# Kernel optimization log

Measured on AMD Instinct MI355X. Metric: run time of the kernel, lower is better.

The kernel has to match this reference:

```python
import jax, jax.numpy as jnp
import numpy as np

NEG_INF = -1e9  # large negative used to mask the H-direction self position (CCNet INF trick)


def _cca(x, q_w, q_b, k_w, k_b, v_w, v_b, gamma):
    # x: [B, C, H, W]
    B, C, H, W = x.shape
    # 1x1 convs are per-pixel channel matmuls
    q = jnp.einsum('oc,bchw->bohw', q_w, x) + q_b[None, :, None, None]  # [B,2,H,W]
    k = jnp.einsum('oc,bchw->bohw', k_w, x) + k_b[None, :, None, None]  # [B,2,H,W]
    v = jnp.einsum('oc,bchw->bohw', v_w, x) + v_b[None, :, None, None]  # [B,16,H,W]

    # column (H-direction) affinities: query (h,w) vs keys (j,w)
    energy_H = jnp.einsum('bchw,bcjw->bhwj', q, k)  # [B,H,W,H]
    diag = jnp.eye(H, dtype=bool)[None, :, None, :]  # mask j == h (self counted once, in W branch)
    energy_H = jnp.where(diag, NEG_INF, energy_H)
    # row (W-direction) affinities: query (h,w) vs keys (h,j)
    energy_W = jnp.einsum('bchw,bchj->bhwj', q, k)  # [B,H,W,W]

    attn = jax.nn.softmax(jnp.concatenate([energy_H, energy_W], axis=3), axis=3)  # [B,H,W,H+W]
    att_H = attn[..., :H]
    att_W = attn[..., H:]

    out_H = jnp.einsum('bhwj,bcjw->bchw', att_H, v)
    out_W = jnp.einsum('bhwj,bchj->bchw', att_W, v)
    return gamma[0] * (out_H + out_W) + x


def setup_inputs() -> dict:
    key = jax.random.key(0)
    ks = jax.random.split(key, 8)
    b, c, d, h, w = 1, 16, 24, 96, 192
    return {
        'cost_volume': jax.random.normal(ks[0], (b, c, d, h, w), jnp.float32),
        'q_w': jax.random.normal(ks[1], (2, 16), jnp.float32) * 0.1,
        'q_b': jax.random.normal(ks[2], (2,), jnp.float32) * 0.1,
        'k_w': jax.random.normal(ks[3], (2, 16), jnp.float32) * 0.1,
        'k_b': jax.random.normal(ks[4], (2,), jnp.float32) * 0.1,
        'v_w': jax.random.normal(ks[5], (16, 16), jnp.float32) * 0.1,
        'v_b': jax.random.normal(ks[6], (16,), jnp.float32) * 0.1,
        'gamma': jax.random.normal(ks[7], (1,), jnp.float32),
    }


def reference(cost_volume, q_w, q_b, k_w, k_b, v_w, v_b, gamma):
    b, c, d, h, w = cost_volume.shape
    # fold disparity into batch: [b,c,d,h,w] -> [b*d, c, h, w]
    x = jnp.transpose(cost_volume, (0, 2, 1, 3, 4)).reshape(b * d, c, h, w)
    x = _cca(x, q_w, q_b, k_w, k_b, v_w, v_b, gamma)
    x = _cca(x, q_w, q_b, k_w, k_b, v_w, v_b, gamma)  # same module applied twice
    return jnp.transpose(x.reshape(b, d, c, h, w), (0, 2, 1, 3, 4))
```

## Files before the change

kernel.cpp:

```cpp
#include <hip/hip_runtime.h>

#define C 16
#define NIMG 24
#define H 96
#define W 192
#define PX (H*W)
#define LOG2E 1.44269504088896f

typedef float v2f  __attribute__((ext_vector_type(2)));
typedef float v4f  __attribute__((ext_vector_type(4)));
typedef short v8s  __attribute__((ext_vector_type(8)));

#define QP_OFF 0
#define KP_OFF (NIMG*PX*2)
#define VB4_OFF (2*NIMG*PX*2)
#define VBP_OFF (VB4_OFF + NIMG*PX*C/2)
#define CMAX_OFF (VBP_OFF + NIMG*PX*C/2)
#define RMAX_OFF (CMAX_OFF + NIMG*2*W)
#define SC_OFF   (RMAX_OFF + NIMG*2*H)
#define ACC_OFF  (SC_OFF + NIMG*PX)

__device__ __forceinline__ unsigned short f2bf(float x) {
    union { float f; unsigned u; } v; v.f = x;
    unsigned r = v.u + 0x7fffu + ((v.u >> 16) & 1u);
    return (unsigned short)(r >> 16);
}
__device__ __forceinline__ float bf2f(unsigned short u) {
    union { unsigned u; float f; } v; v.u = ((unsigned)u) << 16;
    return v.f;
}

__global__ __launch_bounds__(256)
void qkv_kernel(const float* __restrict__ x, long xn_s, long xc_s,
                const float* __restrict__ qw, const float* __restrict__ qb,
                const float* __restrict__ kw, const float* __restrict__ kb,
                const float* __restrict__ vw, const float* __restrict__ vb,
                float2* __restrict__ Qp, float2* __restrict__ Kp,
                ushort4* __restrict__ Vb4, unsigned short* __restrict__ Vbp,
                float* __restrict__ cmax_zero)
{
    __shared__ float wq[2*C+2], wk[2*C+2], wv[C*C+C];
    int tid = threadIdx.x;
    if (tid < 2*C) { wq[tid] = qw[tid]; wk[tid] = kw[tid]; }
    if (tid < 2)   { wq[2*C+tid] = qb[tid]; wk[2*C+tid] = kb[tid]; }
    if (tid < C*C) wv[tid] = vw[tid];
    if (tid < C)   wv[C*C+tid] = vb[tid];

    if (blockIdx.x < 36) {
        int zi = blockIdx.x*256 + tid;
        if (zi < NIMG*2*W) cmax_zero[zi] = 0.0f;
    }
    __syncthreads();

    int id = blockIdx.x*256 + tid;
    int n  = id / PX;
    int p  = id - n*PX;
    int h  = p / W;
    int w  = p - h*W;
    const float* xp = x + (long)n*xn_s + p;

    float xv[C];
    #pragma unroll
    for (int c = 0; c < C; c++) xv[c] = xp[(long)c*xc_s];

    float q0 = wq[2*C], q1 = wq[2*C+1];
    float k0 = wk[2*C], k1 = wk[2*C+1];
    #pragma unroll
    for (int c = 0; c < C; c++) {
        q0 += wq[c]*xv[c];   q1 += wq[C+c]*xv[c];
        k0 += wk[c]*xv[c];   k1 += wk[C+c]*xv[c];
    }
    Qp[id] = make_float2(q0, q1);
    Kp[id] = make_float2(k0, k1);

    float vv[C];
    #pragma unroll
    for (int o = 0; o < C; o++) {
        float a = wv[C*C+o];
        #pragma unroll
        for (int c = 0; c < C; c++) a += wv[o*C+c]*xv[c];
        vv[o] = a;
    }
    unsigned short vb16[C];
    #pragma unroll
    for (int o = 0; o < C; o++) vb16[o] = f2bf(vv[o]);

    #pragma unroll
    for (int c4 = 0; c4 < 4; c4++) {
        ushort4 u;
        u.x = vb16[c4*4+0]; u.y = vb16[c4*4+1];
        u.z = vb16[c4*4+2]; u.w = vb16[c4*4+3];
        Vb4[(((long)n*H + h)*4 + c4)*W + w] = u;
    }
    #pragma unroll
    for (int o = 0; o < C; o++)
        Vbp[(((long)n*H + h)*16 + o)*W + w] = vb16[o];
}

__global__ __launch_bounds__(192)
void stats_kernel(const float2* __restrict__ Kp,
                  float* __restrict__ cmax, float* __restrict__ rmax)
{
    int bid = blockIdx.x;
    int n   = bid >> 2;
    int h0  = (bid & 3) * 24;
    int tid = threadIdx.x;
    const float2* Kpn = Kp + n*PX;

    float c0 = 0.f, c1 = 0.f;
    #pragma unroll 4
    for (int h = 0; h < 24; h++) {
        float2 k = Kpn[(h0+h)*W + tid];
        c0 = fmaxf(c0, fabsf(k.x));
        c1 = fmaxf(c1, fabsf(k.y));
    }
    atomicMax((unsigned*)&cmax[n*2*W + tid],     __float_as_uint(c0));
    atomicMax((unsigned*)&cmax[n*2*W + W + tid], __float_as_uint(c1));

    int r = tid >> 3, seg = tid & 7;
    float r0 = 0.f, r1 = 0.f;
    const float2* kr = Kpn + (h0+r)*W + seg*24;
    #pragma unroll 4
    for (int j = 0; j < 24; j++) {
        float2 k = kr[j];
        r0 = fmaxf(r0, fabsf(k.x));
        r1 = fmaxf(r1, fabsf(k.y));
    }
    r0 = fmaxf(r0, __shfl_xor(r0, 1)); r0 = fmaxf(r0, __shfl_xor(r0, 2)); r0 = fmaxf(r0, __shfl_xor(r0, 4));
    r1 = fmaxf(r1, __shfl_xor(r1, 1)); r1 = fmaxf(r1, __shfl_xor(r1, 2)); r1 = fmaxf(r1, __shfl_xor(r1, 4));
    if (seg == 0) {
        rmax[n*2*H + h0 + r]     = r0;
        rmax[n*2*H + H + h0 + r] = r1;
    }
}

#define VT_WS 1672
__global__ __launch_bounds__(256)
void col_attn_kernel(const float2* __restrict__ Qp, const float2* __restrict__ Kp,
                     const ushort4* __restrict__ Vb4,
                     const float* __restrict__ cmax, const float* __restrict__ rmax,
                     unsigned short* __restrict__ accC, float* __restrict__ sC)
{
    __shared__ unsigned short Vt[4*VT_WS];
    __shared__ unsigned short Ks[4*2*96];
    __shared__ float2         Qs[4*96];
    __shared__ float          Ms[4*96];

    const int chunk = (NIMG*48) / 8;
    int bid = blockIdx.x;
    int swz = (bid & 7)*chunk + (bid >> 3);
    int n   = swz / 48;
    int wg  = swz - n*48;
    int w0  = wg*4;
    int tid = threadIdx.x;

    const float2* Qpn = Qp + n*PX;
    const float2* Kpn = Kp + n*PX;
    const ushort4* Vbn = Vb4 + (long)n*PX*4;

    #pragma unroll
    for (int i = 0; i < 6; i++) {
        int idx = i*256 + tid;
        int wl  = idx & 3;
        int c4  = (idx >> 2) & 3;
        int j   = idx >> 4;
        ushort4 v = Vbn[((long)j*4 + c4)*W + w0 + wl];
        int b = wl*VT_WS + (c4*4)*104 + j;
        Vt[b        ] = v.x;
        Vt[b + 104  ] = v.y;
        Vt[b + 208  ] = v.z;
        Vt[b + 312  ] = v.w;
    }
    #pragma unroll
    for (int i = 0; i < 2; i++) {
        int idx = i*256 + tid;
        if (idx < 384) {
            int wl = idx & 3;
            int j  = idx >> 2;
            float2 kk = Kpn[j*W + w0 + wl];
            Ks[wl*192 + j]      = f2bf(kk.x);
            Ks[wl*192 + 96 + j] = f2bf(kk.y);
        }
    }
    #pragma unroll
    for (int i = 0; i < 2; i++) {
        int idx = i*256 + tid;
        if (idx < 384) {
            int wl = idx & 3;
            int h  = idx >> 2;
            int w  = w0 + wl;
            float2 qq = Qpn[h*W + w];
            float qx = qq.x * LOG2E, qy = qq.y * LOG2E;
            float c0 = cmax[n*2*W + w], c1 = cmax[n*2*W + W + w];
            float r0 = rmax[n*2*H + h], r1 = rmax[n*2*H + H + h];
            float ax = fabsf(qx), ay = fabsf(qy);
            Qs[wl*96 + h] = make_float2(qx, qy);
            Ms[wl*96 + h] = fmaxf(ax*c0 + ay*c1, ax*r0 + ay*r1);
        }
    }
    __syncthreads();

    int wl   = tid >> 6;
    int lane = tid & 63;
    int li   = lane & 15;
    int g    = lane >> 4;
    int w    = w0 + wl;
    unsigned short* accCn = accC + (long)n*PX*16;

    #pragma unroll
    for (int ht = 0; ht < 6; ht++) {
        int hglob = ht*16 + li;
        float2 q = Qs[wl*96 + hglob];
        float  m = Ms[wl*96 + hglob];

        v4f acc = {};
        float sp = 0.f;
        #pragma unroll
        for (int kc = 0; kc < 3; kc++) {
            int j0 = kc*32 + g*8;
            v8s bv = *(const v8s*)&Vt[wl*VT_WS + li*104 + j0];
            v8s kxv = *(const v8s*)&Ks[wl*192 + j0];
            v8s kyv = *(const v8s*)&Ks[wl*192 + 96 + j0];
            v8s af;
            #pragma unroll
            for (int e = 0; e < 8; e++) {
                float e2 = bf2f((unsigned short)kxv[e])*q.x
                         + bf2f((unsigned short)kyv[e])*q.y - m;
                float p = __builtin_amdgcn_exp2f(e2);
                p = (j0 + e == hglob) ? 0.0f : p;
                sp += p;
                af[e] = (short)f2bf(p);
            }
            acc = __builtin_amdgcn_mfma_f32_16x16x32_bf16(af, bv, acc, 0, 0, 0);
        }
        sp += __shfl_xor(sp, 16);
        sp += __shfl_xor(sp, 32);
        if (lane < 16)
            sC[((long)n*H + hglob)*W + w] = sp;

        #pragma unroll
        for (int rr = 0; rr < 4; rr++) {
            int h2 = ht*16 + g*4 + rr;
            accCn[((long)h2*W + w)*16 + li] = f2bf(acc[rr]);
        }
    }
}

__global__ __launch_bounds__(256)
void row_attn_kernel(const float2* __restrict__ Qp, const float2* __restrict__ Kp,
                     const unsigned short* __restrict__ Vbp,
                     const float* __restrict__ cmax, const float* __restrict__ rmax,
                     const unsigned short* __restrict__ accC, const float* __restrict__ sC,
                     const float* __restrict__ xres, long xn_s, long xc_s,
                     float* __restrict__ out, long on_s, long oc_s,
                     const float* __restrict__ gamma_p)
{
    const int chunk = (NIMG*(H/2)) / 8;
    int bid = blockIdx.x;
    int swz = (bid & 7)*chunk + (bid >> 3);
    int n   = swz / (H/2);
    int h0  = (swz - n*(H/2)) * 2;
    int tid = threadIdx.x;

    const float2* Qpn = Qp + n*PX;
    const float*  Kf  = (const float*)(Kp + n*PX);
    const unsigned short* Vrn = Vbp + (long)n*PX*16;

    int wv   = tid >> 6;
    int r    = wv >> 1;
    int half = wv & 1;
    int lane = tid & 63;
    int li   = lane & 15;
    int g    = lane >> 4;
    int h    = h0 + r;

    float r0 = rmax[n*2*H + h], r1 = rmax[n*2*H + H + h];
    float qx[6], qy[6], mW[6];
    #pragma unroll
    for (int t = 0; t < 6; t++) {
        int w = (half*6 + t)*16 + li;
        float2 qq = Qpn[h*W + w];
        float c0 = cmax[n*2*W + w], c1 = cmax[n*2*W + W + w];
        float lqx = qq.x * LOG2E, lqy = qq.y * LOG2E;
        qx[t] = lqx; qy[t] = lqy;
        mW[t] = fmaxf(fabsf(lqx)*c0 + fabsf(lqy)*c1, fabsf(lqx)*r0 + fabsf(lqy)*r1);
    }

    v4f acc[6] = {};
    float sp[6] = {0.f,0.f,0.f,0.f,0.f,0.f};

    const unsigned short* Vrow = Vrn + (long)h*16*W + (long)li*W;
    const float*          Krow = Kf + (long)h*W*2;

    #pragma unroll
    for (int kc = 0; kc < 6; kc++) {
        int j0 = kc*32 + g*8;
        v8s af = *(const v8s*)(Vrow + j0);
        const v4f* kp4 = (const v4f*)(Krow + j0*2);
        v4f k0 = kp4[0], k1 = kp4[1], k2 = kp4[2], k3 = kp4[3];
        float kxv[8] = {k0[0],k0[2],k1[0],k1[2],k2[0],k2[2],k3[0],k3[2]};
        float kyv[8] = {k0[1],k0[3],k1[1],k1[3],k2[1],k2[3],k3[1],k3[3]};
        #pragma unroll
        for (int t = 0; t < 6; t++) {
            v8s bf;
            float sl = sp[t];
            #pragma unroll
            for (int e = 0; e < 8; e++) {
                float ev = qx[t]*kxv[e] + qy[t]*kyv[e];
                float p = __builtin_amdgcn_exp2f(ev - mW[t]);
                sl += p;
                bf[e] = (short)f2bf(p);
            }
            sp[t] = sl;
            acc[t] = __builtin_amdgcn_mfma_f32_16x16x32_bf16(af, bf, acc[t], 0, 0, 0);
        }
    }

    float gam = gamma_p[0];
    #pragma unroll
    for (int t = 0; t < 6; t++) {
        float s = sp[t];
        s += __shfl_xor(s, 16);
        s += __shfl_xor(s, 32);
        int w = (half*6 + t)*16 + li;
        float st = sC[((long)n*H + h)*W + w] + s;
        float inv = 1.0f / st;
        long po = (long)h*W + w;
        const unsigned short* cap = accC + (((long)n*H + h)*W + w)*16 + g*4;
        #pragma unroll
        for (int rr = 0; rr < 4; rr++) {
            int c = g*4 + rr;
            float ac = bf2f(cap[rr]);
            float tot = (acc[t][rr] + ac) * inv;
            out[(long)n*on_s + (long)c*oc_s + po] =
                gam*tot + xres[(long)n*xn_s + (long)c*xc_s + po];
        }
    }
}

extern "C" void kernel_launch(void* const* d_in, const int* in_sizes, int n_in,
                              void* d_out, int out_size, void* d_ws, size_t ws_size,
                              hipStream_t stream) {
    const float* cost = (const float*)d_in[0];
    const float* q_w  = (const float*)d_in[1];
    const float* q_b  = (const float*)d_in[2];
    const float* k_w  = (const float*)d_in[3];
    const float* k_b  = (const float*)d_in[4];
    const float* v_w  = (const float*)d_in[5];
    const float* v_b  = (const float*)d_in[6];
    const float* gamma= (const float*)d_in[7];
    float* out = (float*)d_out;
    float* ws  = (float*)d_ws;

    float2*  Qp = (float2*)(ws + QP_OFF);
    float2*  Kp = (float2*)(ws + KP_OFF);
    ushort4* Vb4 = (ushort4*)(ws + VB4_OFF);
    unsigned short* Vbp = (unsigned short*)(ws + VBP_OFF);
    float*   cm = ws + CMAX_OFF;
    float*   rm = ws + RMAX_OFF;
    float*   sC = ws + SC_OFF;
    unsigned short* aC = (unsigned short*)(ws + ACC_OFF);

    const int qkv_blocks  = (NIMG*PX)/256;
    const int stat_blocks = NIMG*4;
    const int col_blocks  = NIMG*48;
    const int row_blocks  = NIMG*(H/2);

    qkv_kernel<<<qkv_blocks, 256, 0, stream>>>(
        cost, (long)PX, (long)NIMG*PX,
        q_w, q_b, k_w, k_b, v_w, v_b, Qp, Kp, Vb4, Vbp, cm);
    stats_kernel<<<stat_blocks, 192, 0, stream>>>(Kp, cm, rm);
    col_attn_kernel<<<col_blocks, 256, 0, stream>>>(
        Qp, Kp, Vb4, cm, rm, aC, sC);
    row_attn_kernel<<<row_blocks, 256, 0, stream>>>(
        Qp, Kp, Vbp, cm, rm, aC, sC,
        cost, (long)PX, (long)NIMG*PX,
        out,  (long)PX, (long)NIMG*PX,
        gamma);

    qkv_kernel<<<qkv_blocks, 256, 0, stream>>>(
        out, (long)PX, (long)NIMG*PX,
        q_w, q_b, k_w, k_b, v_w, v_b, Qp, Kp, Vb4, Vbp, cm);
    stats_kernel<<<stat_blocks, 192, 0, stream>>>(Kp, cm, rm);
    col_attn_kernel<<<col_blocks, 256, 0, stream>>>(
        Qp, Kp, Vb4, cm, rm, aC, sC);
    row_attn_kernel<<<row_blocks, 256, 0, stream>>>(
        Qp, Kp, Vbp, cm, rm, aC, sC,
        out, (long)PX, (long)NIMG*PX,
        out, (long)PX, (long)NIMG*PX,
        gamma);
}
```

Before: 156.3 us.

## Fuse key-magnitude stats into QKV kernel using per-image global max bound

Drops the separate stats kernel. The QKV kernel now computes a per-image global max of |k| with wave shuffles and atomicMax, and both attention kernels form their softmax shift from that single bound instead of per-row and per-column maxima. The column kernel also stops staging Q and the bound in LDS and reads Q directly from global memory. This trades a coarser, looser exponent shift, which risks exp2 underflow and lost precision when key magnitudes vary a lot, for two fewer launches and less global traffic. The buffer is zeroed only once per call, so the second pass reuses a bound that already includes the first pass's values.

```diff
diff --git a/kernel.cpp b/kernel.cpp
--- a/kernel.cpp
+++ b/kernel.cpp
@@ -15,10 +15,9 @@
 #define KP_OFF (NIMG*PX*2)
 #define VB4_OFF (2*NIMG*PX*2)
 #define VBP_OFF (VB4_OFF + NIMG*PX*C/2)
-#define CMAX_OFF (VBP_OFF + NIMG*PX*C/2)
-#define RMAX_OFF (CMAX_OFF + NIMG*2*W)
-#define SC_OFF   (RMAX_OFF + NIMG*2*H)
-#define ACC_OFF  (SC_OFF + NIMG*PX)
+#define GM_OFF  (VBP_OFF + NIMG*PX*C/2)
+#define SC_OFF  (GM_OFF + 128)
+#define ACC_OFF (SC_OFF + NIMG*PX)
 
 __device__ __forceinline__ unsigned short f2bf(float x) {
     union { float f; unsigned u; } v; v.f = x;
@@ -37,7 +36,7 @@
                 const float* __restrict__ vw, const float* __restrict__ vb,
                 float2* __restrict__ Qp, float2* __restrict__ Kp,
                 ushort4* __restrict__ Vb4, unsigned short* __restrict__ Vbp,
-                float* __restrict__ cmax_zero)
+                float* __restrict__ gm)
 {
     __shared__ float wq[2*C+2], wk[2*C+2], wv[C*C+C];
     int tid = threadIdx.x;
@@ -45,11 +44,6 @@
     if (tid < 2)   { wq[2*C+tid] = qb[tid]; wk[2*C+tid] = kb[tid]; }
     if (tid < C*C) wv[tid] = vw[tid];
     if (tid < C)   wv[C*C+tid] = vb[tid];
-
-    if (blockIdx.x < 36) {
-        int zi = blockIdx.x*256 + tid;
-        if (zi < NIMG*2*W) cmax_zero[zi] = 0.0f;
-    }
     __syncthreads();
 
     int id = blockIdx.x*256 + tid;
@@ -73,6 +67,19 @@
     Qp[id] = make_float2(q0, q1);
     Kp[id] = make_float2(k0, k1);
 
+    {
+        float a0 = fabsf(k0), a1 = fabsf(k1);
+        #pragma unroll
+        for (int d = 1; d < 64; d <<= 1) {
+            a0 = fmaxf(a0, __shfl_xor(a0, d));
+            a1 = fmaxf(a1, __shfl_xor(a1, d));
+        }
+        if ((tid & 63) == 0) {
+            atomicMax((unsigned*)&gm[n*2+0], __float_as_uint(a0));
+            atomicMax((unsigned*)&gm[n*2+1], __float_as_uint(a1));
+        }
+    }
+
     float vv[C];
     #pragma unroll
     for (int o = 0; o < C; o++) {
@@ -97,54 +104,15 @@
         Vbp[(((long)n*H + h)*16 + o)*W + w] = vb16[o];
 }
 
-__global__ __launch_bounds__(192)
-void stats_kernel(const float2* __restrict__ Kp,
-                  float* __restrict__ cmax, float* __restrict__ rmax)
-{
-    int bid = blockIdx.x;
-    int n   = bid >> 2;
-    int h0  = (bid & 3) * 24;
-    int tid = threadIdx.x;
-    const float2* Kpn = Kp + n*PX;
-
-    float c0 = 0.f, c1 = 0.f;
-    #pragma unroll 4
-    for (int h = 0; h < 24; h++) {
-        float2 k = Kpn[(h0+h)*W + tid];
-        c0 = fmaxf(c0, fabsf(k.x));
-        c1 = fmaxf(c1, fabsf(k.y));
-    }
-    atomicMax((unsigned*)&cmax[n*2*W + tid],     __float_as_uint(c0));
-    atomicMax((unsigned*)&cmax[n*2*W + W + tid], __float_as_uint(c1));
-
-    int r = tid >> 3, seg = tid & 7;
-    float r0 = 0.f, r1 = 0.f;
-    const float2* kr = Kpn + (h0+r)*W + seg*24;
-    #pragma unroll 4
-    for (int j = 0; j < 24; j++) {
-        float2 k = kr[j];
-        r0 = fmaxf(r0, fabsf(k.x));
-        r1 = fmaxf(r1, fabsf(k.y));
-    }
-    r0 = fmaxf(r0, __shfl_xor(r0, 1)); r0 = fmaxf(r0, __shfl_xor(r0, 2)); r0 = fmaxf(r0, __shfl_xor(r0, 4));
-    r1 = fmaxf(r1, __shfl_xor(r1, 1)); r1 = fmaxf(r1, __shfl_xor(r1, 2)); r1 = fmaxf(r1, __shfl_xor(r1, 4));
-    if (seg == 0) {
-        rmax[n*2*H + h0 + r]     = r0;
-        rmax[n*2*H + H + h0 + r] = r1;
-    }
-}
-
 #define VT_WS 1672
 __global__ __launch_bounds__(256)
 void col_attn_kernel(const float2* __restrict__ Qp, const float2* __restrict__ Kp,
                      const ushort4* __restrict__ Vb4,
-                     const float* __restrict__ cmax, const float* __restrict__ rmax,
+                     const float* __restrict__ gm,
                      unsigned short* __restrict__ accC, float* __restrict__ sC)
 {
     __shared__ unsigned short Vt[4*VT_WS];
     __shared__ unsigned short Ks[4*2*96];
-    __shared__ float2         Qs[4*96];
-    __shared__ float          Ms[4*96];
 
     const int chunk = (NIMG*48) / 8;
     int bid = blockIdx.x;
@@ -157,6 +125,7 @@
     const float2* Qpn = Qp + n*PX;
     const float2* Kpn = Kp + n*PX;
     const ushort4* Vbn = Vb4 + (long)n*PX*4;
+    float g0 = gm[n*2+0], g1 = gm[n*2+1];
 
     #pragma unroll
     for (int i = 0; i < 6; i++) {
@@ -182,22 +151,6 @@
             Ks[wl*192 + 96 + j] = f2bf(kk.y);
         }
     }
-    #pragma unroll
-    for (int i = 0; i < 2; i++) {
-        int idx = i*256 + tid;
-        if (idx < 384) {
-            int wl = idx & 3;
-            int h  = idx >> 2;
-            int w  = w0 + wl;
-            float2 qq = Qpn[h*W + w];
-            float qx = qq.x * LOG2E, qy = qq.y * LOG2E;
-            float c0 = cmax[n*2*W + w], c1 = cmax[n*2*W + W + w];
-            float r0 = rmax[n*2*H + h], r1 = rmax[n*2*H + H + h];
-            float ax = fabsf(qx), ay = fabsf(qy);
-            Qs[wl*96 + h] = make_float2(qx, qy);
-            Ms[wl*96 + h] = fmaxf(ax*c0 + ay*c1, ax*r0 + ay*r1);
-        }
-    }
     __syncthreads();
 
     int wl   = tid >> 6;
@@ -210,8 +163,9 @@
     #pragma unroll
     for (int ht = 0; ht < 6; ht++) {
         int hglob = ht*16 + li;
-        float2 q = Qs[wl*96 + hglob];
-        float  m = Ms[wl*96 + hglob];
+        float2 qq = Qpn[hglob*W + w];
+        float qx = qq.x * LOG2E, qy = qq.y * LOG2E;
+        float m  = fabsf(qx)*g0 + fabsf(qy)*g1;
 
         v4f acc = {};
         float sp = 0.f;
@@ -224,8 +178,8 @@
             v8s af;
             #pragma unroll
             for (int e = 0; e < 8; e++) {
-                float e2 = bf2f((unsigned short)kxv[e])*q.x
-                         + bf2f((unsigned short)kyv[e])*q.y - m;
+                float e2 = bf2f((unsigned short)kxv[e])*qx
+                         + bf2f((unsigned short)kyv[e])*qy - m;
                 float p = __builtin_amdgcn_exp2f(e2);
                 p = (j0 + e == hglob) ? 0.0f : p;
                 sp += p;
@@ -249,7 +203,7 @@
 __global__ __launch_bounds__(256)
 void row_attn_kernel(const float2* __restrict__ Qp, const float2* __restrict__ Kp,
                      const unsigned short* __restrict__ Vbp,
-                     const float* __restrict__ cmax, const float* __restrict__ rmax,
+                     const float* __restrict__ gm,
                      const unsigned short* __restrict__ accC, const float* __restrict__ sC,
                      const float* __restrict__ xres, long xn_s, long xc_s,
                      float* __restrict__ out, long on_s, long oc_s,
@@ -265,6 +219,7 @@
     const float2* Qpn = Qp + n*PX;
     const float*  Kf  = (const float*)(Kp + n*PX);
     const unsigned short* Vrn = Vbp + (long)n*PX*16;
+    float g0 = gm[n*2+0], g1 = gm[n*2+1];
 
     int wv   = tid >> 6;
     int r    = wv >> 1;
@@ -274,16 +229,14 @@
     int g    = lane >> 4;
     int h    = h0 + r;
 
-    float r0 = rmax[n*2*H + h], r1 = rmax[n*2*H + H + h];
     float qx[6], qy[6], mW[6];
     #pragma unroll
     for (int t = 0; t < 6; t++) {
         int w = (half*6 + t)*16 + li;
         float2 qq = Qpn[h*W + w];
-        float c0 = cmax[n*2*W + w], c1 = cmax[n*2*W + W + w];
         float lqx = qq.x * LOG2E, lqy = qq.y * LOG2E;
         qx[t] = lqx; qy[t] = lqy;
-        mW[t] = fmaxf(fabsf(lqx)*c0 + fabsf(lqy)*c1, fabsf(lqx)*r0 + fabsf(lqy)*r1);
+        mW[t] = fabsf(lqx)*g0 + fabsf(lqy)*g1;
     }
 
     v4f acc[6] = {};
@@ -356,36 +309,34 @@
     float2*  Kp = (float2*)(ws + KP_OFF);
     ushort4* Vb4 = (ushort4*)(ws + VB4_OFF);
     unsigned short* Vbp = (unsigned short*)(ws + VBP_OFF);
-    float*   cm = ws + CMAX_OFF;
-    float*   rm = ws + RMAX_OFF;
+    float*   gm = ws + GM_OFF;
     float*   sC = ws + SC_OFF;
     unsigned short* aC = (unsigned short*)(ws + ACC_OFF);
 
-    const int qkv_blocks  = (NIMG*PX)/256;
-    const int stat_blocks = NIMG*4;
-    const int col_blocks  = NIMG*48;
-    const int row_blocks  = NIMG*(H/2);
+    const int qkv_blocks = (NIMG*PX)/256;
+    const int col_blocks = NIMG*48;
+    const int row_blocks = NIMG*(H/2);
+
+    hipMemsetAsync(gm, 0, 2*NIMG*sizeof(float), stream);
 
     qkv_kernel<<<qkv_blocks, 256, 0, stream>>>(
         cost, (long)PX, (long)NIMG*PX,
-        q_w, q_b, k_w, k_b, v_w, v_b, Qp, Kp, Vb4, Vbp, cm);
-    stats_kernel<<<stat_blocks, 192, 0, stream>>>(Kp, cm, rm);
+        q_w, q_b, k_w, k_b, v_w, v_b, Qp, Kp, Vb4, Vbp, gm);
     col_attn_kernel<<<col_blocks, 256, 0, stream>>>(
-        Qp, Kp, Vb4, cm, rm, aC, sC);
+        Qp, Kp, Vb4, gm, aC, sC);
     row_attn_kernel<<<row_blocks, 256, 0, stream>>>(
-        Qp, Kp, Vbp, cm, rm, aC, sC,
+        Qp, Kp, Vbp, gm, aC, sC,
         cost, (long)PX, (long)NIMG*PX,
         out,  (long)PX, (long)NIMG*PX,
         gamma);
 
     qkv_kernel<<<qkv_blocks, 256, 0, stream>>>(
         out, (long)PX, (long)NIMG*PX,
-        q_w, q_b, k_w, k_b, v_w, v_b, Qp, Kp, Vb4, Vbp, cm);
-    stats_kernel<<<stat_blocks, 192, 0, stream>>>(Kp, cm, rm);
+        q_w, q_b, k_w, k_b, v_w, v_b, Qp, Kp, Vb4, Vbp, gm);
     col_attn_kernel<<<col_blocks, 256, 0, stream>>>(
-        Qp, Kp, Vb4, cm, rm, aC, sC);
+        Qp, Kp, Vb4, gm, aC, sC);
     row_attn_kernel<<<row_blocks, 256, 0, stream>>>(
-        Qp, Kp, Vbp, cm, rm, aC, sC,
+        Qp, Kp, Vbp, gm, aC, sC,
         out, (long)PX, (long)NIMG*PX,
         out, (long)PX, (long)NIMG*PX,
         gamma);
```

Result: slower. 385.3 us (+146.5%).
